# Kernel tuning notes

Measured on AMD Instinct MI355X. Metric: run time of the kernel, lower is better.

Reference implementation:

```python
import jax, jax.numpy as jnp
import numpy as np

D_MODEL = 256
N_LAYERS = 2
EXPAND = 2
D_INNER = EXPAND * D_MODEL  # 512
D_STATE = 16
D_CONV = 4
DT_RANK = max(1, D_MODEL // 16)  # 16


def _selective_scan(x, dt, B, C, A, D):
    # x, dt: [b, l, d]   B, C: [b, l, n]   A: [d, n]   D: [d]
    dA = jnp.exp(jnp.einsum('bld,dn->bldn', dt, A))          # discretized state matrix
    dBx = jnp.einsum('bld,bln,bld->bldn', dt, B, x)           # dt * B * u

    def step(h, inp):
        dA_t, dBx_t, C_t = inp                                 # [b,d,n],[b,d,n],[b,n]
        h = dA_t * h + dBx_t
        y = jnp.einsum('bdn,bn->bd', h, C_t)
        return h, y

    h0 = jnp.zeros((x.shape[0], A.shape[0], A.shape[1]), x.dtype)
    _, ys = jax.lax.scan(step, h0, (jnp.moveaxis(dA, 1, 0),
                                    jnp.moveaxis(dBx, 1, 0),
                                    jnp.moveaxis(C, 1, 0)))
    return jnp.moveaxis(ys, 0, 1) + x * D                      # [b, l, d]


def _mamba_block(z, in_w, conv_w, conv_b, xp_w, dt_w, dt_b, A_log, Dp, out_w):
    b, l, _ = z.shape
    xz = z @ in_w.T                                            # [b, l, 2*d_inner]
    x, gate = jnp.split(xz, 2, axis=-1)
    # causal depthwise conv1d over time
    xt = jnp.transpose(x, (0, 2, 1))                            # [b, d_inner, l]
    xt = jax.lax.conv_general_dilated(
        xt, conv_w[:, None, :], window_strides=(1,),
        padding=[(D_CONV - 1, 0)], feature_group_count=D_INNER)
    x = jax.nn.silu(jnp.transpose(xt, (0, 2, 1)) + conv_b)      # [b, l, d_inner]
    x_dbl = x @ xp_w.T                                          # [b, l, dt_rank + 2*d_state]
    dt, Bm, Cm = jnp.split(x_dbl, [DT_RANK, DT_RANK + D_STATE], axis=-1)
    dt = jax.nn.softplus(dt @ dt_w.T + dt_b)                    # [b, l, d_inner]
    A = -jnp.exp(A_log)                                         # [d_inner, d_state]
    y = _selective_scan(x, dt, Bm, Cm, A, Dp)
    y = y * jax.nn.silu(gate)
    return y @ out_w.T                                          # [b, l, d_model]


def setup_inputs() -> dict:
    key = jax.random.key(0)
    ks = jax.random.split(key, 9)
    B, L = 2, 4096
    z = jax.random.normal(ks[0], (B, L, D_MODEL), jnp.float32)
    s = 0.02
    in_proj_w = jax.random.normal(ks[1], (N_LAYERS, 2 * D_INNER, D_MODEL), jnp.float32) * s
    conv_w = jax.random.normal(ks[2], (N_LAYERS, D_INNER, D_CONV), jnp.float32) * 0.2
    conv_b = jnp.zeros((N_LAYERS, D_INNER), jnp.float32)
    x_proj_w = jax.random.normal(ks[3], (N_LAYERS, DT_RANK + 2 * D_STATE, D_INNER), jnp.float32) * s
    dt_proj_w = jax.random.normal(ks[4], (N_LAYERS, D_INNER, DT_RANK), jnp.float32) * 0.1
    dt_proj_b = jax.random.uniform(ks[5], (N_LAYERS, D_INNER), jnp.float32, -4.0, -2.0)
    A_log = jnp.log(jnp.broadcast_to(jnp.arange(1, D_STATE + 1, dtype=jnp.float32),
                                     (N_LAYERS, D_INNER, D_STATE)))
    D_param = jnp.ones((N_LAYERS, D_INNER), jnp.float32)
    out_proj_w = jax.random.normal(ks[6], (N_LAYERS, D_MODEL, D_INNER), jnp.float32) * s
    return {"z": z, "in_proj_w": in_proj_w, "conv_w": conv_w, "conv_b": conv_b,
            "x_proj_w": x_proj_w, "dt_proj_w": dt_proj_w, "dt_proj_b": dt_proj_b,
            "A_log": A_log, "D_param": D_param, "out_proj_w": out_proj_w}


def reference(z, in_proj_w, conv_w, conv_b, x_proj_w, dt_proj_w, dt_proj_b,
              A_log, D_param, out_proj_w):
    for i in range(N_LAYERS):
        z = _mamba_block(z, in_proj_w[i], conv_w[i], conv_b[i], x_proj_w[i],
                         dt_proj_w[i], dt_proj_b[i], A_log[i], D_param[i], out_proj_w[i])
    return z
```

## Files before the change

kernel.cpp:

```cpp
#include <hip/hip_runtime.h>
#include <hip/hip_bf16.h>
#include <cstdint>
#include <cstddef>

#define DM   256
#define DI   512
#define DS   16
#define LSEQ 4096
#define BATCH 2
#define BLROWS (BATCH * LSEQ)
#define NCH  128
#define CLEN 32
#define XCP  536
#define ZSP  272

#define OFF_XX  0
#define OFF_XD  0
#define OFF_Z   37520
#define OFF_XC  37520
#define SMEM_SZ 71824

typedef __bf16 bf16x8 __attribute__((ext_vector_type(8)));
typedef float  f32x4  __attribute__((ext_vector_type(4)));
typedef unsigned short u16;
typedef u16 u16x8 __attribute__((ext_vector_type(8)));
typedef u16 u16x4 __attribute__((ext_vector_type(4)));

__device__ __forceinline__ u16 f2bfu(float f) {
    union { float f; unsigned u; } c; c.f = f;
    unsigned u = c.u;
    return (u16)((u + 0x7fffu + ((u >> 16) & 1u)) >> 16);
}
__device__ __forceinline__ float bfu2f(u16 u) {
    union { unsigned u; float f; } c; c.u = ((unsigned)u) << 16; return c.f;
}
__device__ __forceinline__ float siluf(float v) {
    return v * (1.0f / (1.0f + __expf(-v)));
}

#define N_INW  (2*1024*256)
#define N_OUTW (2*256*512)
#define N_XPW  (2*64*512)
#define N_Z    (BLROWS*DM)
__global__ __launch_bounds__(256) void cast_all_k(
    const float* __restrict__ in_w, const float* __restrict__ out_w,
    const float* __restrict__ xp_w, const float* __restrict__ z,
    u16* __restrict__ inw_bf, u16* __restrict__ outw_bf,
    u16* __restrict__ xpw_bf, u16* __restrict__ z_bf) {
    int i = blockIdx.x * 256 + threadIdx.x;
    if (i < N_INW) {
        inw_bf[i] = f2bfu(in_w[i]);
    } else if (i < N_INW + N_OUTW) {
        int j = i - N_INW;
        outw_bf[j] = f2bfu(out_w[j]);
    } else if (i < N_INW + N_OUTW + N_XPW) {
        int j = i - (N_INW + N_OUTW);
        int k = j & 511, o = (j >> 9) & 63, l = j >> 15;
        xpw_bf[j] = f2bfu((o < 48) ? xp_w[(l * 48 + o) * 512 + k] : 0.0f);
    } else {
        int j = i - (N_INW + N_OUTW + N_XPW);
        z_bf[j] = f2bfu(z[j]);
    }
}

__global__ __launch_bounds__(512) void fused_a_k(
    const u16* __restrict__ zin, const u16* __restrict__ inw,
    const float* __restrict__ cw, const float* __restrict__ cb,
    const __bf16* __restrict__ xpw,
    const float* __restrict__ dtw, const float* __restrict__ dtb,
    const float* __restrict__ Alog,
    u16* __restrict__ xcb, u16* __restrict__ dtob, u16* __restrict__ gateb,
    float* __restrict__ BCg, u16* __restrict__ Pb, u16* __restrict__ Sb) {
    __shared__ __align__(16) char smem[SMEM_SZ];
    u16*  z_s   = (u16*)(smem + OFF_Z);
    u16*  xx_s  = (u16*)(smem + OFF_XX);
    u16*  xc_s  = (u16*)(smem + OFF_XC);
    float* xd_s = (float*)(smem + OFF_XD);
    int tid = threadIdx.x;
    int c = blockIdx.x, b = blockIdx.y, half = blockIdx.z;
    int bl0 = b * LSEQ + c * CLEN;
    int wave = tid >> 6, lane = tid & 63;
    int row = lane & 15, q = lane >> 4;
    int d = tid;

    for (int idx = tid; idx < 48 * 32; idx += 512) {
        int r = idx >> 5, c8 = idx & 31;
        u16x8 v = {0,0,0,0,0,0,0,0};
        if (r < 35 && (c > 0 || r >= 3))
            v = *(const u16x8*)(zin + (size_t)(bl0 - 3 + r) * DM + c8 * 8);
        *(u16x8*)(z_s + r * ZSP + c8 * 8) = v;
    }
    __syncthreads();

    for (int g = 0; g < 4; ++g) {
        f32x4 acc[3] = {};
        const u16* wp = inw + (size_t)(half*512 + g*128 + wave*16 + row) * 256;
        #pragma unroll
        for (int kb = 0; kb < 8; ++kb) {
            bf16x8 bb = *(const bf16x8*)(wp + kb*32 + q*8);
            #pragma unroll
            for (int mt = 0; mt < 3; ++mt) {
                bf16x8 a = *(const bf16x8*)(z_s + (mt*16 + row) * ZSP + kb*32 + q*8);
                acc[mt] = __builtin_amdgcn_mfma_f32_16x16x32_bf16(a, bb, acc[mt], 0, 0, 0);
            }
        }
        int col = g * 128 + wave * 16 + row;
        #pragma unroll
        for (int mt = 0; mt < 3; ++mt)
            #pragma unroll
            for (int r = 0; r < 4; ++r) {
                int grow = mt * 16 + q * 4 + r;
                if (half == 0) {
                    if (grow < 35) xx_s[grow * XCP + col] = f2bfu(acc[mt][r]);
                } else {
                    int t = grow - 3;
                    if (t >= 0 && t < CLEN)
                        gateb[(size_t)(bl0 + t) * DI + col] = f2bfu(acc[mt][r]);
                }
            }
    }
    if (half == 1) return;
    __syncthreads();

    {
        float w0 = cw[d*4], w1 = cw[d*4+1], w2 = cw[d*4+2], w3 = cw[d*4+3];
        float bias = cb[d];
        float xm3 = bfu2f(xx_s[0*XCP + d]);
        float xm2 = bfu2f(xx_s[1*XCP + d]);
        float xm1 = bfu2f(xx_s[2*XCP + d]);
        #pragma unroll 4
        for (int t = 0; t < CLEN; ++t) {
            float xcur = bfu2f(xx_s[(t + 3) * XCP + d]);
            float v = siluf(fmaf(w0, xm3, fmaf(w1, xm2, fmaf(w2, xm1, fmaf(w3, xcur, bias)))));
            u16 vb = f2bfu(v);
            xc_s[t * XCP + d] = vb;
            xcb[(size_t)(bl0 + t) * DI + d] = vb;
            xm3 = xm2; xm2 = xm1; xm1 = xcur;
        }
    }
    __syncthreads();

    {
        int mt = wave & 1, nt = wave >> 1;
        f32x4 acc = {0.f, 0.f, 0.f, 0.f};
        #pragma unroll
        for (int kb = 0; kb < 16; ++kb) {
            bf16x8 a = *(const bf16x8*)&xc_s[(mt*16 + row) * XCP + kb*32 + q*8];
            bf16x8 bb = *(const bf16x8*)(xpw + (size_t)(nt*16 + row) * 512 + kb*32 + q*8);
            acc = __builtin_amdgcn_mfma_f32_16x16x32_bf16(a, bb, acc, 0, 0, 0);
        }
        #pragma unroll
        for (int r = 0; r < 4; ++r)
            xd_s[(mt*16 + q*4 + r) * 68 + nt*16 + row] = acc[r];
    }
    __syncthreads();

    for (int i = tid; i < CLEN * 32; i += 512) {
        int t = i >> 5, cc = i & 31;
        BCg[((size_t)(b*NCH + c) * CLEN + t) * 32 + cc] = xd_s[t*68 + 16 + cc];
    }

    {
        float dtwr[16];
        const f32x4* w4 = (const f32x4*)(dtw + (size_t)d * 16);
        #pragma unroll
        for (int g = 0; g < 4; ++g) { f32x4 v = w4[g];
            dtwr[g*4] = v[0]; dtwr[g*4+1] = v[1]; dtwr[g*4+2] = v[2]; dtwr[g*4+3] = v[3]; }
        float dtbv = dtb[d];
        float Ac[16];
        const f32x4* a4 = (const f32x4*)(Alog + (size_t)d * 16);
        #pragma unroll
        for (int g = 0; g < 4; ++g) { f32x4 v = a4[g];
            #pragma unroll
            for (int j = 0; j < 4; ++j) Ac[g*4+j] = -__expf(v[j]); }
        bool fastp = true;
        #pragma unroll
        for (int n = 1; n < 16; ++n)
            fastp = fastp && (fabsf(Ac[n] - (float)(n+1) * Ac[0]) <= 1e-4f * fabsf(Ac[n]));
        float p[16], s[16];
        #pragma unroll
        for (int n = 0; n < 16; ++n) { p[n] = 1.0f; s[n] = 0.0f; }
        for (int t = 0; t < CLEN; ++t) {
            float acc = dtbv;
            #pragma unroll
            for (int r = 0; r < 16; ++r) acc = fmaf(xd_s[t*68 + r], dtwr[r], acc);
            float dtv = (acc > 20.0f) ? acc : logf(1.0f + __expf(acc));
            dtob[(size_t)(bl0 + t) * DI + d] = f2bfu(dtv);
            float xv = bfu2f(xc_s[t * XCP + d]);
            float dx = dtv * xv;
            float an[16];
            if (fastp) {
                float a0 = __expf(dtv * Ac[0]);
                an[0] = a0;
                #pragma unroll
                for (int n = 1; n < 16; ++n) an[n] = an[n-1] * a0;
            } else {
                #pragma unroll
                for (int n = 0; n < 16; ++n) an[n] = __expf(dtv * Ac[n]);
            }
            #pragma unroll
            for (int n = 0; n < 16; ++n) {
                s[n] = fmaf(an[n], s[n], xd_s[t*68 + 16 + n] * dx);
                p[n] *= an[n];
            }
        }
        size_t base = ((size_t)(b*NCH + c) * DI + d) * 16;
        u16x8 pv0, pv1, sv0, sv1;
        #pragma unroll
        for (int n = 0; n < 8; ++n) {
            pv0[n] = f2bfu(p[n]);   pv1[n] = f2bfu(p[8+n]);
            sv0[n] = f2bfu(s[n]);   sv1[n] = f2bfu(s[8+n]);
        }
        *(u16x8*)(Pb + base)     = pv0;  *(u16x8*)(Pb + base + 8) = pv1;
        *(u16x8*)(Sb + base)     = sv0;  *(u16x8*)(Sb + base + 8) = sv1;
    }
}

__global__ __launch_bounds__(256) void scanB_k(
    const u16* __restrict__ Pb, const u16* __restrict__ Sb,
    float* __restrict__ H) {
    int i = blockIdx.x * 256 + threadIdx.x;
    int b = i >> 11, j4 = i & 2047;
    f32x4 h = {0.f, 0.f, 0.f, 0.f};
    for (int c = 0; c < NCH; ++c) {
        size_t i4 = (size_t)(b*NCH + c) * 2048 + j4;
        u16x4 pv = ((const u16x4*)Pb)[i4];
        u16x4 sv = ((const u16x4*)Sb)[i4];
        ((f32x4*)H)[i4] = h;
        #pragma unroll
        for (int j = 0; j < 4; ++j) h[j] = fmaf(bfu2f(pv[j]), h[j], bfu2f(sv[j]));
    }
}

__global__ __launch_bounds__(512) void fused_c_k(
    const u16* __restrict__ xcb, const u16* __restrict__ dtob,
    const float* __restrict__ BCg, const float* __restrict__ H,
    const float* __restrict__ Alog, const float* __restrict__ Dp,
    const u16* __restrict__ gateb, const __bf16* __restrict__ outw,
    u16* __restrict__ Ob, float* __restrict__ Of) {
    __shared__ u16 y_s[CLEN * XCP];
    __shared__ float BCs[CLEN * 32];
    int tid = threadIdx.x;
    int c = blockIdx.x, b = blockIdx.y;
    int bl0 = b * LSEQ + c * CLEN;
    int d = tid;

    for (int i = tid; i < CLEN * 32; i += 512)
        BCs[i] = BCg[(size_t)(b*NCH + c) * (CLEN*32) + i];

    float Ac[16], h[16];
    {
        const f32x4* a4 = (const f32x4*)(Alog + (size_t)d * 16);
        const f32x4* h4 = (const f32x4*)(H + ((size_t)(b*NCH + c) * DI + d) * 16);
        #pragma unroll
        for (int g = 0; g < 4; ++g) {
            f32x4 av = a4[g]; f32x4 hv = h4[g];
            #pragma unroll
            for (int j = 0; j < 4; ++j) { Ac[g*4+j] = -__expf(av[j]); h[g*4+j] = hv[j]; }
        }
    }
    bool fastp = true;
    #pragma unroll
    for (int n = 1; n < 16; ++n)
        fastp = fastp && (fabsf(Ac[n] - (float)(n+1) * Ac[0]) <= 1e-4f * fabsf(Ac[n]));
    float Dv = Dp[d];
    __syncthreads();

    #pragma unroll 4
    for (int t = 0; t < CLEN; ++t) {
        float dtv = bfu2f(dtob[(size_t)(bl0 + t) * DI + d]);
        float xv  = bfu2f(xcb[(size_t)(bl0 + t) * DI + d]);
        float gv  = bfu2f(gateb[(size_t)(bl0 + t) * DI + d]);
        float dx = dtv * xv;
        float an[16];
        if (fastp) {
            float a0 = __expf(dtv * Ac[0]);
            an[0] = a0;
            #pragma unroll
            for (int n = 1; n < 16; ++n) an[n] = an[n-1] * a0;
        } else {
            #pragma unroll
            for (int n = 0; n < 16; ++n) an[n] = __expf(dtv * Ac[n]);
        }
        float y = 0.f;
        #pragma unroll
        for (int n = 0; n < 16; ++n) {
            h[n] = fmaf(an[n], h[n], BCs[t*32 + n] * dx);
            y = fmaf(h[n], BCs[t*32 + 16 + n], y);
        }
        float yv = fmaf(xv, Dv, y) * siluf(gv);
        y_s[t * XCP + d] = f2bfu(yv);
    }
    __syncthreads();

    {
        int wave = tid >> 6, lane = tid & 63;
        int row = lane & 15, q = lane >> 4;
        int mt = wave & 1, ng = wave >> 1;
        f32x4 acc[4] = {};
        #pragma unroll
        for (int kb = 0; kb < 16; ++kb) {
            bf16x8 a = *(const bf16x8*)&y_s[(mt*16 + row) * XCP + kb*32 + q*8];
            #pragma unroll
            for (int ni = 0; ni < 4; ++ni) {
                bf16x8 bb = *(const bf16x8*)(outw +
                    (size_t)(ng*64 + ni*16 + row) * 512 + kb*32 + q*8);
                acc[ni] = __builtin_amdgcn_mfma_f32_16x16x32_bf16(a, bb, acc[ni], 0, 0, 0);
            }
        }
        #pragma unroll
        for (int r = 0; r < 4; ++r) {
            size_t gr = (size_t)(bl0 + mt*16 + q*4 + r) * DM;
            #pragma unroll
            for (int ni = 0; ni < 4; ++ni) {
                int gc = ng*64 + ni*16 + row;
                if (Ob) Ob[gr + gc] = f2bfu(acc[ni][r]);
                else    Of[gr + gc] = acc[ni][r];
            }
        }
    }
}

extern "C" void kernel_launch(void* const* d_in, const int* in_sizes, int n_in,
                              void* d_out, int out_size, void* d_ws, size_t ws_size,
                              hipStream_t stream) {
    (void)in_sizes; (void)n_in; (void)out_size; (void)ws_size;
    const float* z_in   = (const float*)d_in[0];
    const float* in_w   = (const float*)d_in[1];
    const float* conv_w = (const float*)d_in[2];
    const float* conv_b = (const float*)d_in[3];
    const float* xp_w   = (const float*)d_in[4];
    const float* dt_w   = (const float*)d_in[5];
    const float* dt_b   = (const float*)d_in[6];
    const float* A_log  = (const float*)d_in[7];
    const float* D_par  = (const float*)d_in[8];
    const float* out_w  = (const float*)d_in[9];
    float* outp = (float*)d_out;

    char* p = (char*)d_ws;
    auto alloc = [&](size_t bytes) { char* r = p; p += (bytes + 255) & ~(size_t)255; return r; };
    u16* z_bf    = (u16*)alloc((size_t)BLROWS*DM*2);
    u16* z2_bf   = (u16*)alloc((size_t)BLROWS*DM*2);
    u16* xc_bf   = (u16*)alloc((size_t)BLROWS*DI*2);
    u16* dt_bf   = (u16*)alloc((size_t)BLROWS*DI*2);
    u16* gate_bf = (u16*)alloc((size_t)BLROWS*DI*2);
    u16* inw_bf  = (u16*)alloc((size_t)2*1024*256*2);
    u16* outw_bf = (u16*)alloc((size_t)2*256*512*2);
    u16* xpw_bf  = (u16*)alloc((size_t)2*64*512*2);
    float* BCg   = (float*)alloc((size_t)BATCH*NCH*CLEN*32*4);
    u16* Pbuf    = (u16*)alloc((size_t)BATCH*NCH*DI*DS*2);
    u16* Sbuf    = (u16*)alloc((size_t)BATCH*NCH*DI*DS*2);
    float* Hbuf  = (float*)alloc((size_t)BATCH*NCH*DI*DS*4);

    cast_all_k<<<(N_INW + N_OUTW + N_XPW + N_Z)/256, 256, 0, stream>>>(
        in_w, out_w, xp_w, z_in, inw_bf, outw_bf, xpw_bf, z_bf);

    const u16* zcur = z_bf;
    for (int l = 0; l < 2; ++l) {
        fused_a_k<<<dim3(NCH, BATCH, 2), 512, 0, stream>>>(
            zcur, inw_bf + (size_t)l*1024*256,
            conv_w + (size_t)l*DI*4, conv_b + (size_t)l*DI,
            (const __bf16*)(xpw_bf + (size_t)l*64*512),
            dt_w + (size_t)l*DI*16, dt_b + (size_t)l*DI,
            A_log + (size_t)l*DI*DS,
            xc_bf, dt_bf, gate_bf, BCg, Pbuf, Sbuf);
        scanB_k<<<16, 256, 0, stream>>>(Pbuf, Sbuf, Hbuf);
        fused_c_k<<<dim3(NCH, BATCH), 512, 0, stream>>>(
            xc_bf, dt_bf, BCg, Hbuf,
            A_log + (size_t)l*DI*DS, D_par + (size_t)l*DI,
            gate_bf, (const __bf16*)(outw_bf + (size_t)l*256*512),
            (l == 0) ? z2_bf : nullptr, (l == 1) ? outp : nullptr);
        zcur = z2_bf;
    }
}
```

Before: 261.4 us.

## Halve chunk length to 16 and split K across waves in small GEMMs

Cuts the per-block time chunk from 32 to 16 rows, doubling the number of chunks and blocks and reducing shared memory per block. Because a 16-row chunk fills only one MFMA M-tile, the x_proj and out_proj GEMMs now split the K dimension between wave halves and combine the partial sums through shared memory. The aim is more blocks and occupancy, and more parallelism in the chunked scan. In exchange the 3-row conv halo is recomputed relative to fewer rows, the scan's cross-chunk combine has twice as many chunks, and extra syncs are added.

```diff
diff --git a/kernel.cpp b/kernel.cpp
--- a/kernel.cpp
+++ b/kernel.cpp
@@ -9,16 +9,16 @@
 #define LSEQ 4096
 #define BATCH 2
 #define BLROWS (BATCH * LSEQ)
-#define NCH  128
-#define CLEN 32
+#define NCH  256
+#define CLEN 16
 #define XCP  536
 #define ZSP  272
 
 #define OFF_XX  0
 #define OFF_XD  0
-#define OFF_Z   37520
-#define OFF_XC  37520
-#define SMEM_SZ 71824
+#define OFF_Z   20368
+#define OFF_XC  20368
+#define SMEM_SZ 37776
 
 typedef __bf16 bf16x8 __attribute__((ext_vector_type(8)));
 typedef float  f32x4  __attribute__((ext_vector_type(4)));
@@ -83,35 +83,35 @@
     int row = lane & 15, q = lane >> 4;
     int d = tid;
 
-    for (int idx = tid; idx < 48 * 32; idx += 512) {
+    for (int idx = tid; idx < 32 * 32; idx += 512) {
         int r = idx >> 5, c8 = idx & 31;
         u16x8 v = {0,0,0,0,0,0,0,0};
-        if (r < 35 && (c > 0 || r >= 3))
+        if (r < 19 && (c > 0 || r >= 3))
             v = *(const u16x8*)(zin + (size_t)(bl0 - 3 + r) * DM + c8 * 8);
         *(u16x8*)(z_s + r * ZSP + c8 * 8) = v;
     }
     __syncthreads();
 
     for (int g = 0; g < 4; ++g) {
-        f32x4 acc[3] = {};
+        f32x4 acc[2] = {};
         const u16* wp = inw + (size_t)(half*512 + g*128 + wave*16 + row) * 256;
         #pragma unroll
         for (int kb = 0; kb < 8; ++kb) {
             bf16x8 bb = *(const bf16x8*)(wp + kb*32 + q*8);
             #pragma unroll
-            for (int mt = 0; mt < 3; ++mt) {
+            for (int mt = 0; mt < 2; ++mt) {
                 bf16x8 a = *(const bf16x8*)(z_s + (mt*16 + row) * ZSP + kb*32 + q*8);
                 acc[mt] = __builtin_amdgcn_mfma_f32_16x16x32_bf16(a, bb, acc[mt], 0, 0, 0);
             }
         }
         int col = g * 128 + wave * 16 + row;
         #pragma unroll
-        for (int mt = 0; mt < 3; ++mt)
+        for (int mt = 0; mt < 2; ++mt)
             #pragma unroll
             for (int r = 0; r < 4; ++r) {
                 int grow = mt * 16 + q * 4 + r;
                 if (half == 0) {
-                    if (grow < 35) xx_s[grow * XCP + col] = f2bfu(acc[mt][r]);
+                    if (grow < 19) xx_s[grow * XCP + col] = f2bfu(acc[mt][r]);
                 } else {
                     int t = grow - 3;
                     if (t >= 0 && t < CLEN)
@@ -141,17 +141,25 @@
     __syncthreads();
 
     {
-        int mt = wave & 1, nt = wave >> 1;
+        int nt = wave & 3, kh = wave >> 2;
         f32x4 acc = {0.f, 0.f, 0.f, 0.f};
         #pragma unroll
-        for (int kb = 0; kb < 16; ++kb) {
-            bf16x8 a = *(const bf16x8*)&xc_s[(mt*16 + row) * XCP + kb*32 + q*8];
-            bf16x8 bb = *(const bf16x8*)(xpw + (size_t)(nt*16 + row) * 512 + kb*32 + q*8);
+        for (int kb = 0; kb < 8; ++kb) {
+            bf16x8 a = *(const bf16x8*)&xc_s[row * XCP + kh*256 + kb*32 + q*8];
+            bf16x8 bb = *(const bf16x8*)(xpw + (size_t)(nt*16 + row) * 512 + kh*256 + kb*32 + q*8);
             acc = __builtin_amdgcn_mfma_f32_16x16x32_bf16(a, bb, acc, 0, 0, 0);
         }
-        #pragma unroll
-        for (int r = 0; r < 4; ++r)
-            xd_s[(mt*16 + q*4 + r) * 68 + nt*16 + row] = acc[r];
+        if (kh == 0) {
+            #pragma unroll
+            for (int r = 0; r < 4; ++r)
+                xd_s[(q*4 + r) * 68 + nt*16 + row] = acc[r];
+        }
+        __syncthreads();
+        if (kh == 1) {
+            #pragma unroll
+            for (int r = 0; r < 4; ++r)
+                xd_s[(q*4 + r) * 68 + nt*16 + row] += acc[r];
+        }
     }
     __syncthreads();
 
@@ -296,26 +304,39 @@
     {
         int wave = tid >> 6, lane = tid & 63;
         int row = lane & 15, q = lane >> 4;
-        int mt = wave & 1, ng = wave >> 1;
+        int ng = wave & 3, kh = wave >> 2;
         f32x4 acc[4] = {};
         #pragma unroll
-        for (int kb = 0; kb < 16; ++kb) {
-            bf16x8 a = *(const bf16x8*)&y_s[(mt*16 + row) * XCP + kb*32 + q*8];
+        for (int kb = 0; kb < 8; ++kb) {
+            bf16x8 a = *(const bf16x8*)&y_s[row * XCP + kh*256 + kb*32 + q*8];
             #pragma unroll
             for (int ni = 0; ni < 4; ++ni) {
                 bf16x8 bb = *(const bf16x8*)(outw +
-                    (size_t)(ng*64 + ni*16 + row) * 512 + kb*32 + q*8);
+                    (size_t)(ng*64 + ni*16 + row) * 512 + kh*256 + kb*32 + q*8);
                 acc[ni] = __builtin_amdgcn_mfma_f32_16x16x32_bf16(a, bb, acc[ni], 0, 0, 0);
             }
         }
-        #pragma unroll
-        for (int r = 0; r < 4; ++r) {
-            size_t gr = (size_t)(bl0 + mt*16 + q*4 + r) * DM;
-            #pragma unroll
-            for (int ni = 0; ni < 4; ++ni) {
-                int gc = ng*64 + ni*16 + row;
-                if (Ob) Ob[gr + gc] = f2bfu(acc[ni][r]);
-                else    Of[gr + gc] = acc[ni][r];
+        float* part = (float*)y_s;
+        __syncthreads();
+        if (kh == 0) {
+            #pragma unroll
+            for (int r = 0; r < 4; ++r)
+                #pragma unroll
+                for (int ni = 0; ni < 4; ++ni)
+                    part[(q*4 + r) * 256 + ng*64 + ni*16 + row] = acc[ni][r];
+        }
+        __syncthreads();
+        if (kh == 1) {
+            #pragma unroll
+            for (int r = 0; r < 4; ++r) {
+                size_t gr = (size_t)(bl0 + q*4 + r) * DM;
+                #pragma unroll
+                for (int ni = 0; ni < 4; ++ni) {
+                    int gc = ng*64 + ni*16 + row;
+                    float v = part[(q*4 + r) * 256 + gc] + acc[ni][r];
+                    if (Ob) Ob[gr + gc] = f2bfu(v);
+                    else    Of[gr + gc] = v;
+                }
             }
         }
     }
```

After: 289.6 us. 10.8% more time.
